# Performance work log

Measured on AMD Instinct MI355X. Metric: run time of the kernel, lower is better.

The kernel has to match this reference:

```python
import jax, jax.numpy as jnp
import numpy as np
from jax import lax

K_NN = 3
LN_EPS = 1e-5


def _encode(x, W1, b1, W2, b2, W3, b3, gamma, beta):
    h = jax.nn.relu(x @ W1 + b1)
    h = jax.nn.relu(h @ W2 + b2)
    z = h @ W3 + b3
    mu = jnp.mean(z, axis=-1, keepdims=True)
    var = jnp.mean((z - mu) ** 2, axis=-1, keepdims=True)  # biased var, as torch LayerNorm
    return (z - mu) / jnp.sqrt(var + LN_EPS) * gamma + beta


def _state_entropy(src, tgt, k):
    # pairwise L2 distance via GEMM formulation (same math as torch.norm of diffs)
    sq = (jnp.sum(src * src, -1)[:, None]
          + jnp.sum(tgt * tgt, -1)[None, :]
          - 2.0 * (src @ tgt.T))
    dists = jnp.sqrt(jnp.maximum(sq, 0.0))  # [N_src, N_tgt]
    # sum of k smallest distances (kthvalue 1..k), single fused top-k
    neg_k, _ = lax.top_k(-dists, k)
    knn = jnp.sum(-neg_k, axis=-1)
    # faithful to the source bug: loop variable shadows k, final divisor is k-1
    knn = knn / float(k - 1)
    return knn[:, None]


def setup_inputs() -> dict:
    key = jax.random.key(0)
    ks = jax.random.split(key, 6)
    N, D, H, L = 16384, 128, 256, 256
    return {
        "state_src": jax.random.normal(ks[0], (N, D), jnp.float32),
        "state_tgt": jax.random.normal(ks[1], (N, D), jnp.float32),
        "W1": jax.random.normal(ks[2], (D, H), jnp.float32) * 0.05,
        "b1": jnp.zeros((H,), jnp.float32),
        "W2": jax.random.normal(ks[3], (H, H), jnp.float32) * 0.05,
        "b2": jnp.zeros((H,), jnp.float32),
        "W3": jax.random.normal(ks[4], (H, L), jnp.float32) * 0.05,
        "b3": jnp.zeros((L,), jnp.float32),
        "gamma": jnp.ones((L,), jnp.float32),
        "beta": jnp.zeros((L,), jnp.float32),
    }


def reference(state_src, state_tgt, W1, b1, W2, b2, W3, b3, gamma, beta):
    src = _encode(state_src, W1, b1, W2, b2, W3, b3, gamma, beta)  # forward()
    tgt = _encode(state_tgt, W1, b1, W2, b2, W3, b3, gamma, beta)
    entropy = _state_entropy(src, tgt, K_NN)  # compute_state_entropy (no_grad)
    return src, entropy
```

## Files before the change

### kernel.cpp

```cpp
#include <hip/hip_runtime.h>
#include <math.h>


typedef __attribute__((ext_vector_type(8))) short short8;
typedef __attribute__((ext_vector_type(4))) float floatx4;
typedef __attribute__((ext_vector_type(8))) int int8v;

#define MFMA16(a, b, c) __builtin_amdgcn_mfma_f32_16x16x32_bf16((a), (b), (c), 0, 0, 0)

__device__ __forceinline__ floatx4 mfma8(int8v a, int8v b, floatx4 c) {
  return __builtin_amdgcn_mfma_scale_f32_16x16x128_f8f6f4(a, b, c, 0, 0, 0, 0x7F, 0, 0x7F);
}

static const size_t OFF_W1F  = 0;
static const size_t OFF_W2F  = 65536;
static const size_t OFF_W3F  = 196608;
static const size_t OFF_SRCF = 327680;
static const size_t OFF_TGTF = 327680 + 8388608;
static const size_t OFF_S2   = 327680 + 2 * 8388608;
static const size_t OFF_T2   = OFF_S2 + 65536;
static const size_t OFF_P    = OFF_T2 + 65536;
static const size_t OFF_SRC8 = 18808832;
static const size_t OFF_TGT8 = 18808832 + 4194304;
static const size_t WS_NEED  = OFF_TGT8 + 4194304;

__device__ __forceinline__ unsigned short f2bf(float f) {
  unsigned int u = __float_as_uint(f);
  return (unsigned short)((u + 0x7FFFu + ((u >> 16) & 1u)) >> 16);
}

__device__ __forceinline__ unsigned int pkbf(float lo, float hi) {
  unsigned int r;
  asm("v_cvt_pk_bf16_f32 %0, %1, %2" : "=v"(r) : "v"(lo), "v"(hi));
  return r;
}

__device__ __forceinline__ void ins3(float& t0, float& t1, float& t2, float v) {
  float n0 = fminf(t0, v);
  float n1 = __builtin_amdgcn_fmed3f(t0, t1, v);
  float n2 = __builtin_amdgcn_fmed3f(t1, t2, v);
  t0 = n0; t1 = n1; t2 = n2;
}

__device__ __forceinline__ void gload16(const void* g, void* l) {
  __builtin_amdgcn_global_load_lds(
      (const __attribute__((address_space(1))) unsigned int*)(unsigned long long)(uintptr_t)g,
      (__attribute__((address_space(3))) unsigned int*)(unsigned int)(uintptr_t)l, 16, 0, 0);
}

__device__ __forceinline__ unsigned int sxor(unsigned int v, int m) {
  return (unsigned int)__shfl_xor((int)v, m, 64);
}

__device__ __forceinline__ void exchange8(const unsigned int* p0, const unsigned int* p1,
                                          short8* frag, int g) {
  const bool go = (g & 1), gh = (g >> 1);
#pragma unroll
  for (int ks = 0; ks < 8; ++ks) {
    unsigned int a_o = p0[2 * ks], b_o = p1[2 * ks];
    unsigned int c_o = p0[2 * ks + 1], d_o = p1[2 * ks + 1];
    unsigned int a_n = sxor(a_o, 16), b_n = sxor(b_o, 16);
    unsigned int c_n = sxor(c_o, 16), d_n = sxor(d_o, 16);
    unsigned int qab0 = go ? a_n : a_o, qab1 = go ? b_n : b_o;
    unsigned int qab2 = go ? a_o : a_n, qab3 = go ? b_o : b_n;
    unsigned int qcd0 = go ? c_n : c_o, qcd1 = go ? d_n : d_o;
    unsigned int qcd2 = go ? c_o : c_n, qcd3 = go ? d_o : d_n;
    unsigned int s0 = gh ? qab0 : qcd0, s1 = gh ? qab1 : qcd1;
    unsigned int s2 = gh ? qab2 : qcd2, s3 = gh ? qab3 : qcd3;
    unsigned int r0 = sxor(s0, 32), r1 = sxor(s1, 32);
    unsigned int r2 = sxor(s2, 32), r3 = sxor(s3, 32);
    union { unsigned int u[4]; short8 s; } cv;
    cv.u[0] = (g == 0) ? qab0 : (g == 3) ? qcd0 : r0;
    cv.u[1] = (g == 0) ? qab1 : (g == 3) ? qcd1 : r1;
    cv.u[2] = (g == 0) ? qab2 : (g == 3) ? qcd2 : r2;
    cv.u[3] = (g == 0) ? qab3 : (g == 3) ? qcd3 : r3;
    frag[ks] = cv.s;
  }
}

__global__ void prep_weights(const float* __restrict__ W1, const float* __restrict__ W2,
                             const float* __restrict__ W3, unsigned short* __restrict__ ws16) {
  int t = blockIdx.x * 256 + threadIdx.x;
  const float* W;
  unsigned short* dst;
  int f, ksbits;
  if (t < 4096)       { W = W1; dst = ws16 + OFF_W1F / 2; f = t;         ksbits = 2; }
  else if (t < 12288) { W = W2; dst = ws16 + OFF_W2F / 2; f = t - 4096;  ksbits = 3; }
  else                { W = W3; dst = ws16 + OFF_W3F / 2; f = t - 12288; ksbits = 3; }
  int l  = f & 63;
  int fk = f >> 6;
  int ks = fk & ((1 << ksbits) - 1);
  int cf = fk >> ksbits;
  int k0 = ks * 32 + ((l >> 4) << 3);
  int c  = (cf << 4) + (l & 15);
  short8 v;
#pragma unroll
  for (int j = 0; j < 8; ++j) v[j] = (short)f2bf(W[(size_t)(k0 + j) * 256 + c]);
  *(short8*)(dst + (size_t)f * 8) = v;
}

__global__ __launch_bounds__(256, 2) void encode_kernel(
    const float* __restrict__ xsrc, const float* __restrict__ xtgt,
    const float* __restrict__ b1, const float* __restrict__ b2, const float* __restrict__ b3,
    const float* __restrict__ gamma, const float* __restrict__ beta,
    float* __restrict__ out_src, unsigned short* __restrict__ ws16) {
  __shared__ unsigned short wlds[2][16384];
  const int tid = threadIdx.x, w = tid >> 6, l = tid & 63;
  const int dr = l & 15, g = l >> 4;
  const int blk = blockIdx.x;
  const bool is_src = blk < 256;
  const int row0 = ((blk & 255) << 6) + (w << 4);
  const int row = row0 + dr;
  const float* __restrict__ X = is_src ? xsrc : xtgt;
  unsigned short* __restrict__ fragout = ws16 + (is_src ? OFF_SRCF / 2 : OFF_TGTF / 2);
  float* __restrict__ nrm = (float*)(ws16 + (is_src ? OFF_S2 / 2 : OFF_T2 / 2));
  const unsigned short* W1f = ws16 + OFF_W1F / 2;
  const unsigned short* W2f = ws16 + OFF_W2F / 2;
  const unsigned short* W3f = ws16 + OFF_W3F / 2;

  auto stageW = [&](int bsel, int q) {
    const unsigned short* src;
    int rounds;
    if (q < 4)      { src = W1f + q * 8192;        rounds = 4; }
    else if (q < 8) { src = W2f + (q - 4) * 16384; rounds = 8; }
    else            { src = W3f + (q - 8) * 16384; rounds = 8; }
#pragma unroll
    for (int r = 0; r < 8; ++r) {
      if (r < rounds)
        gload16(src + r * 2048 + w * 512 + l * 8, &wlds[bsel][r * 2048 + w * 512]);
    }
  };

  short8 xf[4];
  const float* xr = X + (size_t)row * 128;
#pragma unroll
  for (int ks = 0; ks < 4; ++ks) {
    floatx4 f0 = *(const floatx4*)(xr + ks * 32 + g * 8);
    floatx4 f1 = *(const floatx4*)(xr + ks * 32 + g * 8 + 4);
    union { unsigned int u[4]; short8 s; } cv;
    cv.u[0] = pkbf(f0[0], f0[1]); cv.u[1] = pkbf(f0[2], f0[3]);
    cv.u[2] = pkbf(f1[0], f1[1]); cv.u[3] = pkbf(f1[2], f1[3]);
    xf[ks] = cv.s;
  }

  unsigned int p0[16], p1[16];
  short8 hf[8];

  stageW(0, 0);
  __syncthreads();
  int cur = 0;

#pragma unroll
  for (int qq = 0; qq < 4; ++qq) {
    stageW(cur ^ 1, qq + 1);
#pragma unroll
    for (int i = 0; i < 4; ++i) {
      int cf = qq * 4 + i;
      floatx4 acc = {0.f, 0.f, 0.f, 0.f};
#pragma unroll
      for (int ks = 0; ks < 4; ++ks) {
        short8 wf = *(const short8*)(&wlds[cur][((i * 4 + ks) * 64 + l) * 8]);
        acc = MFMA16(wf, xf[ks], acc);
      }
      floatx4 bv = *(const floatx4*)(b1 + cf * 16 + g * 4);
      float h0 = fmaxf(acc[0] + bv[0], 0.f), h1v = fmaxf(acc[1] + bv[1], 0.f);
      float h2v = fmaxf(acc[2] + bv[2], 0.f), h3v = fmaxf(acc[3] + bv[3], 0.f);
      p0[cf] = pkbf(h0, h1v); p1[cf] = pkbf(h2v, h3v);
    }
    __syncthreads();
    cur ^= 1;
  }
  exchange8(p0, p1, hf, g);

#pragma unroll
  for (int qq = 0; qq < 4; ++qq) {
    stageW(cur ^ 1, 5 + qq);
#pragma unroll
    for (int i = 0; i < 4; ++i) {
      int cf = qq * 4 + i;
      floatx4 acc = {0.f, 0.f, 0.f, 0.f};
#pragma unroll
      for (int ks = 0; ks < 8; ++ks) {
        short8 wf = *(const short8*)(&wlds[cur][((i * 8 + ks) * 64 + l) * 8]);
        acc = MFMA16(wf, hf[ks], acc);
      }
      floatx4 bv = *(const floatx4*)(b2 + cf * 16 + g * 4);
      float h0 = fmaxf(acc[0] + bv[0], 0.f), h1v = fmaxf(acc[1] + bv[1], 0.f);
      float h2v = fmaxf(acc[2] + bv[2], 0.f), h3v = fmaxf(acc[3] + bv[3], 0.f);
      p0[cf] = pkbf(h0, h1v); p1[cf] = pkbf(h2v, h3v);
    }
    __syncthreads();
    cur ^= 1;
  }
  exchange8(p0, p1, hf, g);

  floatx4 z[16];
#pragma unroll
  for (int qq = 0; qq < 4; ++qq) {
    if (qq < 3) stageW(cur ^ 1, 9 + qq);
#pragma unroll
    for (int i = 0; i < 4; ++i) {
      int cf = qq * 4 + i;
      floatx4 acc = {0.f, 0.f, 0.f, 0.f};
#pragma unroll
      for (int ks = 0; ks < 8; ++ks) {
        short8 wf = *(const short8*)(&wlds[cur][((i * 8 + ks) * 64 + l) * 8]);
        acc = MFMA16(wf, hf[ks], acc);
      }
      floatx4 bv = *(const floatx4*)(b3 + cf * 16 + g * 4);
#pragma unroll
      for (int j = 0; j < 4; ++j) acc[j] += bv[j];
      z[cf] = acc;
    }
    __syncthreads();
    cur ^= 1;
  }

  float s = 0.f, q = 0.f;
#pragma unroll
  for (int cf = 0; cf < 16; ++cf)
#pragma unroll
    for (int j = 0; j < 4; ++j) { float v = z[cf][j]; s += v; q = fmaf(v, v, q); }
  s += __shfl_xor(s, 16, 64); s += __shfl_xor(s, 32, 64);
  q += __shfl_xor(q, 16, 64); q += __shfl_xor(q, 32, 64);
  float mu = s * 0.00390625f;
  float var = q * 0.00390625f - mu * mu;
  float rstd = rsqrtf(var + 1e-5f);

  const float sc = is_src ? -2.0f : 1.0f;
  float nacc = 0.f;
#pragma unroll
  for (int cf = 0; cf < 16; ++cf) {
    floatx4 gv = *(const floatx4*)(gamma + cf * 16 + g * 4);
    floatx4 bev = *(const floatx4*)(beta + cf * 16 + g * 4);
    float y0 = (z[cf][0] - mu) * rstd * gv[0] + bev[0];
    float y1 = (z[cf][1] - mu) * rstd * gv[1] + bev[1];
    float y2 = (z[cf][2] - mu) * rstd * gv[2] + bev[2];
    float y3 = (z[cf][3] - mu) * rstd * gv[3] + bev[3];
    nacc = fmaf(y0, y0, nacc); nacc = fmaf(y1, y1, nacc);
    nacc = fmaf(y2, y2, nacc); nacc = fmaf(y3, y3, nacc);
    p0[cf] = pkbf(sc * y0, sc * y1); p1[cf] = pkbf(sc * y2, sc * y3);
  }
  nacc += __shfl_xor(nacc, 16, 64); nacc += __shfl_xor(nacc, 32, 64);
  if (g == 0) nrm[row] = nacc;

  short8 yf[8];
  exchange8(p0, p1, yf, g);

  const int tile = row0 >> 4;
#pragma unroll
  for (int ks = 0; ks < 8; ++ks)
    *(short8*)(fragout + ((size_t)(tile * 8 + ks) * 64 + l) * 8) = yf[ks];

  if (is_src) {
    float* orow = out_src + (size_t)row * 256;
#pragma unroll
    for (int ks = 0; ks < 8; ++ks) {
      union { short8 s; unsigned int u[4]; } cv; cv.s = yf[ks];
      floatx4 o0, o1;
      o0[0] = __uint_as_float(cv.u[0] << 16) * -0.5f;
      o0[1] = __uint_as_float(cv.u[0] & 0xffff0000u) * -0.5f;
      o0[2] = __uint_as_float(cv.u[1] << 16) * -0.5f;
      o0[3] = __uint_as_float(cv.u[1] & 0xffff0000u) * -0.5f;
      o1[0] = __uint_as_float(cv.u[2] << 16) * -0.5f;
      o1[1] = __uint_as_float(cv.u[2] & 0xffff0000u) * -0.5f;
      o1[2] = __uint_as_float(cv.u[3] << 16) * -0.5f;
      o1[3] = __uint_as_float(cv.u[3] & 0xffff0000u) * -0.5f;
      *(floatx4*)(orow + ks * 32 + g * 8) = o0;
      *(floatx4*)(orow + ks * 32 + g * 8 + 4) = o1;
    }
  }
}

__global__ __launch_bounds__(256) void repack_fp8(const unsigned short* __restrict__ ws16,
                                                  unsigned char* __restrict__ wsb) {
  int t = blockIdx.x * 256 + threadIdx.x;
  const int side = t >> 17;
  const int u = t & 131071;
  const int df = u >> 6, l = u & 63;
  const int tile = df >> 1, ks2 = df & 1;
  const unsigned short* sbase = ws16 + (side ? OFF_TGTF / 2 : OFF_SRCF / 2);
  unsigned char* dbase = wsb + (side ? OFF_TGT8 : OFF_SRC8);
  int8v r;
#pragma unroll
  for (int sub = 0; sub < 4; ++sub) {
    int sf = (tile * 8 + ks2 * 4 + (l >> 4)) * 64 + sub * 16 + (l & 15);
    short8 v = *(const short8*)(sbase + (size_t)sf * 8);
    float f[8];
#pragma unroll
    for (int j = 0; j < 8; ++j)
      f[j] = __uint_as_float(((unsigned int)(unsigned short)v[j]) << 16);
    unsigned int w0 = __builtin_amdgcn_cvt_pk_fp8_f32(f[0], f[1], 0, 0);
    w0 = __builtin_amdgcn_cvt_pk_fp8_f32(f[2], f[3], w0, 1);
    unsigned int w1 = __builtin_amdgcn_cvt_pk_fp8_f32(f[4], f[5], 0, 0);
    w1 = __builtin_amdgcn_cvt_pk_fp8_f32(f[6], f[7], w1, 1);
    r[sub * 2] = (int)w0;
    r[sub * 2 + 1] = (int)w1;
  }
  *(int8v*)(dbase + ((size_t)df * 64 + l) * 32) = r;
}

__global__ __launch_bounds__(512, 2) void dist8_kernel(
    const unsigned char* __restrict__ src8, const unsigned char* __restrict__ tgt8,
    const float* __restrict__ t2, float* __restrict__ part) {
  __shared__ unsigned char buf[2][32768];
  const int tid = threadIdx.x, w = tid >> 6, l = tid & 63;
  const int blk = blockIdx.x;
  const int split = blk & 7;
  const int rtile = blk >> 3;
  const int R0 = rtile * 512 + w * 64;
  const int C0 = split * 2048;

  int8v a[4][2];
#pragma unroll
  for (int rf = 0; rf < 4; ++rf)
#pragma unroll
    for (int ks2 = 0; ks2 < 2; ++ks2)
      a[rf][ks2] = *(const int8v*)(src8 + (((size_t)(R0 / 16 + rf) * 2 + ks2) * 64 + l) * 32);

  float t3[4][4][3];
#pragma unroll
  for (int rf = 0; rf < 4; ++rf)
#pragma unroll
    for (int j = 0; j < 4; ++j) { t3[rf][j][0] = 1e30f; t3[rf][j][1] = 1e30f; t3[rf][j][2] = 1e30f; }

  const unsigned char* gb0 = tgt8 + (size_t)(C0 / 16) * 2 * 2048;
#define STAGE(bsel, t)                                                        \
  {                                                                           \
    const unsigned char* gb = gb0 + (size_t)(t) * 32768;                      \
    _Pragma("unroll") for (int i = 0; i < 4; ++i) {                           \
      int chunk = w * 4 + i;                                                  \
      gload16(gb + chunk * 1024 + l * 16, &buf[bsel][chunk * 1024]);          \
    }                                                                         \
  }

  STAGE(0, 0);
  float t2v[8];
#pragma unroll
  for (int c = 0; c < 8; ++c) t2v[c] = t2[C0 + c * 16 + (l & 15)];
  __syncthreads();

  for (int t = 0; t < 16; ++t) {
    int cur = t & 1;
    if (t < 15) STAGE(cur ^ 1, t + 1);
    float t2n[8];
    if (t < 15) {
      int nb = C0 + (t + 1) * 128;
#pragma unroll
      for (int c = 0; c < 8; ++c) t2n[c] = t2[nb + c * 16 + (l & 15)];
    }
#pragma unroll
    for (int cf = 0; cf < 8; ++cf) {
      const unsigned char* bb = &buf[cur][cf * 4096];
      int8v b0 = *(const int8v*)(bb + l * 32);
      int8v b1 = *(const int8v*)(bb + 2048 + l * 32);
      float tv = t2v[cf];
      floatx4 acc[4];
#pragma unroll
      for (int rf = 0; rf < 4; ++rf) acc[rf] = (floatx4){tv, tv, tv, tv};
      __builtin_amdgcn_s_setprio(1);
#pragma unroll
      for (int rf = 0; rf < 4; ++rf) acc[rf] = mfma8(a[rf][0], b0, acc[rf]);
#pragma unroll
      for (int rf = 0; rf < 4; ++rf) acc[rf] = mfma8(a[rf][1], b1, acc[rf]);
      __builtin_amdgcn_s_setprio(0);
#pragma unroll
      for (int rf = 0; rf < 4; ++rf)
#pragma unroll
        for (int j = 0; j < 4; ++j)
          ins3(t3[rf][j][0], t3[rf][j][1], t3[rf][j][2], acc[rf][j]);
    }
#pragma unroll
    for (int c = 0; c < 8; ++c) t2v[c] = t2n[c];
    __syncthreads();
  }
#undef STAGE

#pragma unroll
  for (int rf = 0; rf < 4; ++rf)
#pragma unroll
    for (int j = 0; j < 4; ++j)
#pragma unroll
      for (int m = 1; m < 16; m <<= 1) {
        float o0 = __shfl_xor(t3[rf][j][0], m, 64);
        float o1 = __shfl_xor(t3[rf][j][1], m, 64);
        float o2 = __shfl_xor(t3[rf][j][2], m, 64);
        ins3(t3[rf][j][0], t3[rf][j][1], t3[rf][j][2], o0);
        ins3(t3[rf][j][0], t3[rf][j][1], t3[rf][j][2], o1);
        ins3(t3[rf][j][0], t3[rf][j][1], t3[rf][j][2], o2);
      }
  if ((l & 15) == 0) {
    int q = l >> 4;
#pragma unroll
    for (int rf = 0; rf < 4; ++rf)
#pragma unroll
      for (int j = 0; j < 4; ++j) {
        int row = R0 + rf * 16 + q * 4 + j;
        float* p = part + ((size_t)row * 8 + split) * 3;
        p[0] = t3[rf][j][0];
        p[1] = t3[rf][j][1];
        p[2] = t3[rf][j][2];
      }
  }
}

__global__ __launch_bounds__(512, 2) void dist_kernel(
    const unsigned short* __restrict__ srcf, const unsigned short* __restrict__ tgtf,
    const float* __restrict__ t2, float* __restrict__ part) {
  __shared__ unsigned short buf[2][32768];
  const int tid = threadIdx.x, w = tid >> 6, l = tid & 63;
  const int blk = blockIdx.x;
  const int split = blk & 7;
  const int rtile = blk >> 3;
  const int R0 = rtile * 512 + w * 64;
  const int C0 = split * 2048;

  short8 a[4][8];
#pragma unroll
  for (int rf = 0; rf < 4; ++rf)
#pragma unroll
    for (int ks = 0; ks < 8; ++ks)
      a[rf][ks] = *(const short8*)(srcf + (((size_t)(R0 / 16 + rf) * 8 + ks) * 64 + l) * 8);

  float t3[4][4][3];
#pragma unroll
  for (int rf = 0; rf < 4; ++rf)
#pragma unroll
    for (int j = 0; j < 4; ++j) { t3[rf][j][0] = 1e30f; t3[rf][j][1] = 1e30f; t3[rf][j][2] = 1e30f; }

  const unsigned short* gb0 = tgtf + (size_t)(C0 / 16) * 4096;
#define STAGE(bsel, t)                                                        \
  {                                                                           \
    const unsigned short* gb = gb0 + (size_t)(t) * 32768;                     \
    _Pragma("unroll") for (int i = 0; i < 8; ++i) {                           \
      int chunk = w * 8 + i;                                                  \
      gload16(gb + chunk * 512 + l * 8, &buf[bsel][chunk * 512]);             \
    }                                                                         \
  }

  STAGE(0, 0);
  float t2v[8];
#pragma unroll
  for (int c = 0; c < 8; ++c) t2v[c] = t2[C0 + c * 16 + (l & 15)];
  __syncthreads();

  for (int t = 0; t < 16; ++t) {
    int cur = t & 1;
    if (t < 15) STAGE(cur ^ 1, t + 1);
    float t2n[8];
    if (t < 15) {
      int nb = C0 + (t + 1) * 128;
#pragma unroll
      for (int c = 0; c < 8; ++c) t2n[c] = t2[nb + c * 16 + (l & 15)];
    }
#pragma unroll
    for (int cf = 0; cf < 8; ++cf) {
      const unsigned short* bb = &buf[cur][cf << 12];
      float tv = t2v[cf];
      floatx4 acc[4];
      short8 bc = *(const short8*)(bb + l * 8);
#pragma unroll
      for (int rf = 0; rf < 4; ++rf) acc[rf] = (floatx4){tv, tv, tv, tv};
      __builtin_amdgcn_s_setprio(1);
#pragma unroll
      for (int ks = 0; ks < 8; ++ks) {
        short8 bn = bc;
        if (ks < 7) bn = *(const short8*)(bb + (ks + 1) * 512 + l * 8);
#pragma unroll
        for (int rf = 0; rf < 4; ++rf) acc[rf] = MFMA16(a[rf][ks], bc, acc[rf]);
        bc = bn;
      }
      __builtin_amdgcn_s_setprio(0);
#pragma unroll
      for (int rf = 0; rf < 4; ++rf)
#pragma unroll
        for (int j = 0; j < 4; ++j)
          ins3(t3[rf][j][0], t3[rf][j][1], t3[rf][j][2], acc[rf][j]);
    }
#pragma unroll
    for (int c = 0; c < 8; ++c) t2v[c] = t2n[c];
    __syncthreads();
  }
#undef STAGE

#pragma unroll
  for (int rf = 0; rf < 4; ++rf)
#pragma unroll
    for (int j = 0; j < 4; ++j)
#pragma unroll
      for (int m = 1; m < 16; m <<= 1) {
        float o0 = __shfl_xor(t3[rf][j][0], m, 64);
        float o1 = __shfl_xor(t3[rf][j][1], m, 64);
        float o2 = __shfl_xor(t3[rf][j][2], m, 64);
        ins3(t3[rf][j][0], t3[rf][j][1], t3[rf][j][2], o0);
        ins3(t3[rf][j][0], t3[rf][j][1], t3[rf][j][2], o1);
        ins3(t3[rf][j][0], t3[rf][j][1], t3[rf][j][2], o2);
      }
  if ((l & 15) == 0) {
    int q = l >> 4;
#pragma unroll
    for (int rf = 0; rf < 4; ++rf)
#pragma unroll
      for (int j = 0; j < 4; ++j) {
        int row = R0 + rf * 16 + q * 4 + j;
        float* p = part + ((size_t)row * 8 + split) * 3;
        p[0] = t3[rf][j][0];
        p[1] = t3[rf][j][1];
        p[2] = t3[rf][j][2];
      }
  }
}

__global__ void merge_kernel(const float* __restrict__ part, const float* __restrict__ s2,
                             float* __restrict__ eout) {
  int r = blockIdx.x * 256 + threadIdx.x;
  const float* p = part + (size_t)r * 24;
  float u0 = 1e30f, u1 = 1e30f, u2 = 1e30f;
#pragma unroll
  for (int i = 0; i < 24; ++i) ins3(u0, u1, u2, p[i]);
  float sv = s2[r];
  float d0 = sqrtf(fmaxf(sv + u0, 0.f));
  float d1 = sqrtf(fmaxf(sv + u1, 0.f));
  float d2 = sqrtf(fmaxf(sv + u2, 0.f));
  eout[r] = (d0 + d1 + d2) * 0.5f;
}

extern "C" void kernel_launch(void* const* d_in, const int* in_sizes, int n_in,
                              void* d_out, int out_size, void* d_ws, size_t ws_size,
                              hipStream_t stream) {
  const float* xsrc = (const float*)d_in[0];
  const float* xtgt = (const float*)d_in[1];
  const float* W1 = (const float*)d_in[2];
  const float* b1 = (const float*)d_in[3];
  const float* W2 = (const float*)d_in[4];
  const float* b2 = (const float*)d_in[5];
  const float* W3 = (const float*)d_in[6];
  const float* b3 = (const float*)d_in[7];
  const float* gm = (const float*)d_in[8];
  const float* bt = (const float*)d_in[9];
  float* out = (float*)d_out;
  unsigned short* ws16 = (unsigned short*)d_ws;
  unsigned char* wsb = (unsigned char*)d_ws;

  prep_weights<<<80, 256, 0, stream>>>(W1, W2, W3, ws16);
  encode_kernel<<<512, 256, 0, stream>>>(xsrc, xtgt, b1, b2, b3, gm, bt, out, ws16);
  if (ws_size >= WS_NEED) {
    repack_fp8<<<1024, 256, 0, stream>>>(ws16, wsb);
    dist8_kernel<<<256, 512, 0, stream>>>(wsb + OFF_SRC8, wsb + OFF_TGT8,
                                          (const float*)(wsb + OFF_T2),
                                          (float*)(wsb + OFF_P));
  } else {
    dist_kernel<<<256, 512, 0, stream>>>(ws16 + OFF_SRCF / 2, ws16 + OFF_TGTF / 2,
                                         (const float*)(wsb + OFF_T2),
                                         (float*)(wsb + OFF_P));
  }
  merge_kernel<<<64, 256, 0, stream>>>((const float*)(wsb + OFF_P),
                                       (const float*)(wsb + OFF_S2),
                                       out + 4194304);
}
```

Baseline: 120.6 us.

## Split fp8 fragments into 16-byte halves, stage t2 in LDS, use 256-thread blocks

The fp8 repack now stores each 32-byte lane fragment as two 16-byte halves 1024 bytes apart. LDS and global reads become contiguous 16-byte-per-lane accesses, which should cut LDS bank conflicts on the B-fragment loads. The per-tile t2 norms are preloaded once into shared memory instead of being prefetched into registers every iteration. The distance kernel moves from 256 blocks of 512 threads to 512 blocks of 256 threads, so each wave stages twice as many chunks, and the per-block LDS footprint grows.

```diff
diff --git a/kernel.cpp b/kernel.cpp
--- a/kernel.cpp
+++ b/kernel.cpp
@@ -5,11 +5,16 @@
 typedef __attribute__((ext_vector_type(8))) short short8;
 typedef __attribute__((ext_vector_type(4))) float floatx4;
 typedef __attribute__((ext_vector_type(8))) int int8v;
+typedef __attribute__((ext_vector_type(4))) int int4v;
 
 #define MFMA16(a, b, c) __builtin_amdgcn_mfma_f32_16x16x32_bf16((a), (b), (c), 0, 0, 0)
 
 __device__ __forceinline__ floatx4 mfma8(int8v a, int8v b, floatx4 c) {
   return __builtin_amdgcn_mfma_scale_f32_16x16x128_f8f6f4(a, b, c, 0, 0, 0, 0x7F, 0, 0x7F);
+}
+
+__device__ __forceinline__ int8v cat8(int4v lo, int4v hi) {
+  return __builtin_shufflevector(lo, hi, 0, 1, 2, 3, 4, 5, 6, 7);
 }
 
 static const size_t OFF_W1F  = 0;
@@ -281,7 +286,7 @@
   const int tile = df >> 1, ks2 = df & 1;
   const unsigned short* sbase = ws16 + (side ? OFF_TGTF / 2 : OFF_SRCF / 2);
   unsigned char* dbase = wsb + (side ? OFF_TGT8 : OFF_SRC8);
-  int8v r;
+  int r[8];
 #pragma unroll
   for (int sub = 0; sub < 4; ++sub) {
     int sf = (tile * 8 + ks2 * 4 + (l >> 4)) * 64 + sub * 16 + (l & 15);
@@ -297,26 +302,41 @@
     r[sub * 2] = (int)w0;
     r[sub * 2 + 1] = (int)w1;
   }
-  *(int8v*)(dbase + ((size_t)df * 64 + l) * 32) = r;
-}
-
-__global__ __launch_bounds__(512, 2) void dist8_kernel(
+  int4v rlo = {r[0], r[1], r[2], r[3]};
+  int4v rhi = {r[4], r[5], r[6], r[7]};
+  *(int4v*)(dbase + (size_t)df * 2048 + l * 16) = rlo;
+  *(int4v*)(dbase + (size_t)df * 2048 + 1024 + l * 16) = rhi;
+}
+
+__global__ __launch_bounds__(256, 2) void dist8_kernel(
     const unsigned char* __restrict__ src8, const unsigned char* __restrict__ tgt8,
     const float* __restrict__ t2, float* __restrict__ part) {
   __shared__ unsigned char buf[2][32768];
+  __shared__ float t2l[2048];
   const int tid = threadIdx.x, w = tid >> 6, l = tid & 63;
   const int blk = blockIdx.x;
   const int split = blk & 7;
   const int rtile = blk >> 3;
-  const int R0 = rtile * 512 + w * 64;
+  const int R0 = rtile * 256 + w * 64;
   const int C0 = split * 2048;
 
+  {
+    floatx4 v0 = *(const floatx4*)(t2 + C0 + tid * 8);
+    floatx4 v1 = *(const floatx4*)(t2 + C0 + tid * 8 + 4);
+    *(floatx4*)(t2l + tid * 8) = v0;
+    *(floatx4*)(t2l + tid * 8 + 4) = v1;
+  }
+
   int8v a[4][2];
 #pragma unroll
   for (int rf = 0; rf < 4; ++rf)
 #pragma unroll
-    for (int ks2 = 0; ks2 < 2; ++ks2)
-      a[rf][ks2] = *(const int8v*)(src8 + (((size_t)(R0 / 16 + rf) * 2 + ks2) * 64 + l) * 32);
+    for (int ks2 = 0; ks2 < 2; ++ks2) {
+      const unsigned char* ab = src8 + ((size_t)((R0 >> 4) + rf) * 2 + ks2) * 2048;
+      int4v lo = *(const int4v*)(ab + l * 16);
+      int4v hi = *(const int4v*)(ab + 1024 + l * 16);
+      a[rf][ks2] = cat8(lo, hi);
+    }
 
   float t3[4][4][3];
 #pragma unroll
@@ -324,37 +344,31 @@
 #pragma unroll
     for (int j = 0; j < 4; ++j) { t3[rf][j][0] = 1e30f; t3[rf][j][1] = 1e30f; t3[rf][j][2] = 1e30f; }
 
-  const unsigned char* gb0 = tgt8 + (size_t)(C0 / 16) * 2 * 2048;
+  const unsigned char* gb0 = tgt8 + (size_t)(C0 >> 4) * 4096;
 #define STAGE(bsel, t)                                                        \
   {                                                                           \
     const unsigned char* gb = gb0 + (size_t)(t) * 32768;                      \
-    _Pragma("unroll") for (int i = 0; i < 4; ++i) {                           \
-      int chunk = w * 4 + i;                                                  \
+    _Pragma("unroll") for (int i = 0; i < 8; ++i) {                           \
+      int chunk = w * 8 + i;                                                  \
       gload16(gb + chunk * 1024 + l * 16, &buf[bsel][chunk * 1024]);          \
     }                                                                         \
   }
 
   STAGE(0, 0);
-  float t2v[8];
-#pragma unroll
-  for (int c = 0; c < 8; ++c) t2v[c] = t2[C0 + c * 16 + (l & 15)];
   __syncthreads();
 
   for (int t = 0; t < 16; ++t) {
     int cur = t & 1;
     if (t < 15) STAGE(cur ^ 1, t + 1);
-    float t2n[8];
-    if (t < 15) {
-      int nb = C0 + (t + 1) * 128;
-#pragma unroll
-      for (int c = 0; c < 8; ++c) t2n[c] = t2[nb + c * 16 + (l & 15)];
-    }
 #pragma unroll
     for (int cf = 0; cf < 8; ++cf) {
       const unsigned char* bb = &buf[cur][cf * 4096];
-      int8v b0 = *(const int8v*)(bb + l * 32);
-      int8v b1 = *(const int8v*)(bb + 2048 + l * 32);
-      float tv = t2v[cf];
+      int4v l0 = *(const int4v*)(bb + l * 16);
+      int4v h0 = *(const int4v*)(bb + 1024 + l * 16);
+      int4v l1 = *(const int4v*)(bb + 2048 + l * 16);
+      int4v h1 = *(const int4v*)(bb + 3072 + l * 16);
+      int8v b0 = cat8(l0, h0), b1 = cat8(l1, h1);
+      float tv = t2l[t * 128 + cf * 16 + (l & 15)];
       floatx4 acc[4];
 #pragma unroll
       for (int rf = 0; rf < 4; ++rf) acc[rf] = (floatx4){tv, tv, tv, tv};
@@ -370,8 +384,6 @@
         for (int j = 0; j < 4; ++j)
           ins3(t3[rf][j][0], t3[rf][j][1], t3[rf][j][2], acc[rf][j]);
     }
-#pragma unroll
-    for (int c = 0; c < 8; ++c) t2v[c] = t2n[c];
     __syncthreads();
   }
 #undef STAGE
@@ -546,7 +558,7 @@
   encode_kernel<<<512, 256, 0, stream>>>(xsrc, xtgt, b1, b2, b3, gm, bt, out, ws16);
   if (ws_size >= WS_NEED) {
     repack_fp8<<<1024, 256, 0, stream>>>(ws16, wsb);
-    dist8_kernel<<<256, 512, 0, stream>>>(wsb + OFF_SRC8, wsb + OFF_TGT8,
+    dist8_kernel<<<512, 256, 0, stream>>>(wsb + OFF_SRC8, wsb + OFF_TGT8,
                                           (const float*)(wsb + OFF_T2),
                                           (float*)(wsb + OFF_P));
   } else {
```

New measurement: 120.5 us (median of 2 runs). About the same (-0.1%).
